# Kernel optimization log

Hardware: AMD Instinct MI355X
Metric: run time of the kernel (lower is better)

Reference implementation:

```python
import jax, jax.numpy as jnp
import numpy as np

VOCAB, D = 32000, 128
B, R, C, T = 8, 100, 64, 32


def setup_inputs() -> dict:
    key = jax.random.key(0)
    k1, k2, k3 = jax.random.split(key, 3)
    x = jax.random.randint(k1, (B, R, C, T), 0, VOCAB, dtype=jnp.int32)
    W_embed = jax.random.normal(k2, (VOCAB, D), dtype=jnp.float32)
    w_pred = jax.random.normal(k3, (1, D), dtype=jnp.float32) * (1.0 / np.sqrt(D))
    b_pred = jnp.zeros((1,), dtype=jnp.float32)
    return {"x": x, "W_embed": W_embed, "w_pred": w_pred, "b_pred": b_pred}


def reference(x, W_embed, w_pred, b_pred):
    # Embedding gather for every cell token at once: [B,R,C,T,D]
    emb = W_embed[x]
    # Mean over tokens within each cell: [B,R,C,D]
    pooled = emb.mean(axis=-2)
    # Dropout is identity in eval mode. Exact (erf) GELU as in torch nn.GELU default.
    act = jax.nn.gelu(pooled, approximate=False)
    # Linear(D -> 1), squeeze to scalar per cell: [B,R,C]
    out = jnp.einsum('brcd,d->brc', act, w_pred[0]) + b_pred[0]
    return out
```

## Files before the change

kernel.cpp:

```cpp
#include <hip/hip_runtime.h>
#include <math.h>
#include <string.h>

constexpr int VOCAB  = 32000;
constexpr int D      = 128;
constexpr int T      = 32;
constexpr int NCELLS = 8 * 100 * 64;
constexpr int WAVES_PER_BLOCK = 4;

__device__ inline ushort f2bf(float f) {
    uint32_t u;
    memcpy(&u, &f, 4);
    u += 0x7FFFu + ((u >> 16) & 1u);
    return (ushort)(u >> 16);
}
__device__ inline float bf2f(ushort h) {
    uint32_t u = ((uint32_t)h) << 16;
    float f;
    memcpy(&f, &u, 4);
    return f;
}

__global__ __launch_bounds__(256) void convert_W_kernel(
    const float* __restrict__ W, ushort* __restrict__ Wb)
{
    const int i = blockIdx.x * blockDim.x + threadIdx.x;
    float4 v = reinterpret_cast<const float4*>(W)[i];
    ushort4 o;
    o.x = f2bf(v.x);
    o.y = f2bf(v.y);
    o.z = f2bf(v.z);
    o.w = f2bf(v.w);
    reinterpret_cast<ushort4*>(Wb)[i] = o;
}

__global__ __launch_bounds__(256) void gather_kernel(
    const int*    __restrict__ x,
    const ushort* __restrict__ Wb,
    const float*  __restrict__ w_pred,
    const float*  __restrict__ b_pred,
    float*        __restrict__ out)
{
    const int wave = threadIdx.x >> 6;
    const int lane = threadIdx.x & 63;
    const int cell = blockIdx.x * WAVES_PER_BLOCK + wave;
    if (cell >= NCELLS) return;

    const int c    = lane & 31;
    const int half = lane >> 5;

    int myidx = x[(long)cell * T + c];

    float a0 = 0.f, a1 = 0.f, a2 = 0.f, a3 = 0.f;
    #pragma unroll
    for (int t = 0; t < T / 2; ++t) {
        int row = __shfl(myidx, 2 * t + half, 64);
        ushort4 v = reinterpret_cast<const ushort4*>(Wb + (size_t)row * D)[c];
        a0 += bf2f(v.x);
        a1 += bf2f(v.y);
        a2 += bf2f(v.z);
        a3 += bf2f(v.w);
    }
    a0 += __shfl_xor(a0, 32, 64);
    a1 += __shfl_xor(a1, 32, 64);
    a2 += __shfl_xor(a2, 32, 64);
    a3 += __shfl_xor(a3, 32, 64);

    const float inv_t = 1.0f / (float)T;
    a0 *= inv_t; a1 *= inv_t; a2 *= inv_t; a3 *= inv_t;

    const float is2 = 0.70710678118654752440f;
    float g0 = 0.5f * a0 * (1.0f + erff(a0 * is2));
    float g1 = 0.5f * a1 * (1.0f + erff(a1 * is2));
    float g2 = 0.5f * a2 * (1.0f + erff(a2 * is2));
    float g3 = 0.5f * a3 * (1.0f + erff(a3 * is2));

    float4 wv = reinterpret_cast<const float4*>(w_pred)[c];
    float s = g0 * wv.x + g1 * wv.y + g2 * wv.z + g3 * wv.w;

    #pragma unroll
    for (int off = 16; off >= 1; off >>= 1)
        s += __shfl_xor(s, off, 64);

    if (lane == 0)
        out[cell] = s + b_pred[0];
}

extern "C" void kernel_launch(void* const* d_in, const int* in_sizes, int n_in,
                              void* d_out, int out_size, void* d_ws, size_t ws_size,
                              hipStream_t stream) {
    const int*   x      = (const int*)  d_in[0];
    const float* W      = (const float*)d_in[1];
    const float* w_pred = (const float*)d_in[2];
    const float* b_pred = (const float*)d_in[3];
    float*       out    = (float*)d_out;
    ushort*      Wb     = (ushort*)d_ws;

    const int conv_groups = VOCAB * D / 4;
    convert_W_kernel<<<conv_groups / 256, 256, 0, stream>>>(W, Wb);

    const int blocks = (NCELLS + WAVES_PER_BLOCK - 1) / WAVES_PER_BLOCK;
    gather_kernel<<<blocks, 256, 0, stream>>>(x, Wb, w_pred, b_pred, out);
}
```

Before: 106.4 us.

## Split embedding dim into chunk-major bf16 table and combine partial cells atomically

The bf16 embedding table is re-laid out as four chunk-major slices of 32 columns each. Every block now handles one column chunk for a pair of cell groups, so concurrently running blocks read the same compact slice and should get better L2/MALL locality. Partial dot products are combined with atomicAdd into an output that is zeroed by an added memset. This costs four times as many blocks, repeated token-index loads and shuffles, and atomics whose summation order is nondeterministic.

```diff
diff --git a/kernel.cpp b/kernel.cpp
--- a/kernel.cpp
+++ b/kernel.cpp
@@ -6,7 +6,8 @@
 constexpr int D      = 128;
 constexpr int T      = 32;
 constexpr int NCELLS = 8 * 100 * 64;
-constexpr int WAVES_PER_BLOCK = 4;
+constexpr int NCHUNK = 4;
+constexpr int CDIM   = D / NCHUNK;
 
 __device__ inline ushort f2bf(float f) {
     uint32_t u;
@@ -25,13 +26,15 @@
     const float* __restrict__ W, ushort* __restrict__ Wb)
 {
     const int i = blockIdx.x * blockDim.x + threadIdx.x;
-    float4 v = reinterpret_cast<const float4*>(W)[i];
+    const int v = i >> 5;
+    const int k = i & 31;
+    const int chunk = k >> 3;
+    const int sub   = k & 7;
+
+    float4 src = reinterpret_cast<const float4*>(W)[i];
     ushort4 o;
-    o.x = f2bf(v.x);
-    o.y = f2bf(v.y);
-    o.z = f2bf(v.z);
-    o.w = f2bf(v.w);
-    reinterpret_cast<ushort4*>(Wb)[i] = o;
+    o.x = f2bf(src.x); o.y = f2bf(src.y); o.z = f2bf(src.z); o.w = f2bf(src.w);
+    reinterpret_cast<ushort4*>(Wb)[(size_t)chunk * (VOCAB * 8) + (size_t)v * 8 + sub] = o;
 }
 
 __global__ __launch_bounds__(256) void gather_kernel(
@@ -43,47 +46,52 @@
 {
     const int wave = threadIdx.x >> 6;
     const int lane = threadIdx.x & 63;
-    const int cell = blockIdx.x * WAVES_PER_BLOCK + wave;
-    if (cell >= NCELLS) return;
 
-    const int c    = lane & 31;
-    const int half = lane >> 5;
+    const int slot  = blockIdx.x & 7;
+    const int chunk = slot >> 1;
+    const int g     = blockIdx.x >> 3;
+    const int cell  = ((g << 1) + (slot & 1)) * 4 + wave;
 
-    int myidx = x[(long)cell * T + c];
+    const int h = lane & 15;
+    const int q = lane >> 4;
 
-    float a0 = 0.f, a1 = 0.f, a2 = 0.f, a3 = 0.f;
+    int myidx = __builtin_nontemporal_load(x + (size_t)cell * T + (lane & 31));
+
+    const ushort2* __restrict__ base =
+        reinterpret_cast<const ushort2*>(Wb + (size_t)chunk * VOCAB * CDIM);
+
+    float a0 = 0.f, a1 = 0.f;
     #pragma unroll
-    for (int t = 0; t < T / 2; ++t) {
-        int row = __shfl(myidx, 2 * t + half, 64);
-        ushort4 v = reinterpret_cast<const ushort4*>(Wb + (size_t)row * D)[c];
+    for (int i = 0; i < T / 4; ++i) {
+        int row = __shfl(myidx, i * 4 + q, 64);
+        ushort2 v = base[(size_t)row * (CDIM / 2) + h];
         a0 += bf2f(v.x);
         a1 += bf2f(v.y);
-        a2 += bf2f(v.z);
-        a3 += bf2f(v.w);
     }
     a0 += __shfl_xor(a0, 32, 64);
     a1 += __shfl_xor(a1, 32, 64);
-    a2 += __shfl_xor(a2, 32, 64);
-    a3 += __shfl_xor(a3, 32, 64);
+    a0 += __shfl_xor(a0, 16, 64);
+    a1 += __shfl_xor(a1, 16, 64);
 
     const float inv_t = 1.0f / (float)T;
-    a0 *= inv_t; a1 *= inv_t; a2 *= inv_t; a3 *= inv_t;
+    float p0 = a0 * inv_t;
+    float p1 = a1 * inv_t;
 
     const float is2 = 0.70710678118654752440f;
-    float g0 = 0.5f * a0 * (1.0f + erff(a0 * is2));
-    float g1 = 0.5f * a1 * (1.0f + erff(a1 * is2));
-    float g2 = 0.5f * a2 * (1.0f + erff(a2 * is2));
-    float g3 = 0.5f * a3 * (1.0f + erff(a3 * is2));
+    float g0 = 0.5f * p0 * (1.0f + erff(p0 * is2));
+    float g1 = 0.5f * p1 * (1.0f + erff(p1 * is2));
 
-    float4 wv = reinterpret_cast<const float4*>(w_pred)[c];
-    float s = g0 * wv.x + g1 * wv.y + g2 * wv.z + g3 * wv.w;
+    float2 wv = reinterpret_cast<const float2*>(w_pred)[chunk * (CDIM / 2) + h];
+    float s = g0 * wv.x + g1 * wv.y;
 
     #pragma unroll
-    for (int off = 16; off >= 1; off >>= 1)
+    for (int off = 8; off >= 1; off >>= 1)
         s += __shfl_xor(s, off, 64);
 
-    if (lane == 0)
-        out[cell] = s + b_pred[0];
+    if (lane == 0) {
+        if (chunk == 0) s += b_pred[0];
+        atomicAdd(&out[cell], s);
+    }
 }
 
 extern "C" void kernel_launch(void* const* d_in, const int* in_sizes, int n_in,
@@ -99,6 +107,7 @@
     const int conv_groups = VOCAB * D / 4;
     convert_W_kernel<<<conv_groups / 256, 256, 0, stream>>>(W, Wb);
 
-    const int blocks = (NCELLS + WAVES_PER_BLOCK - 1) / WAVES_PER_BLOCK;
-    gather_kernel<<<blocks, 256, 0, stream>>>(x, Wb, w_pred, b_pred, out);
+    hipMemsetAsync(out, 0, (size_t)NCELLS * sizeof(float), stream);
+
+    gather_kernel<<<NCHUNK * (NCELLS / 4), 256, 0, stream>>>(x, Wb, w_pred, b_pred, out);
 }
```

After: 136.1 us. 28.0% more time.
